# Kernel optimization log

Measured on AMD Instinct MI355X. Metric: run time of the kernel, lower is better.

Reference implementation:

```python
import jax, jax.numpy as jnp
import numpy as np

TEMPERATURE = 0.05
EPS = 1e-8  # torch.cosine_similarity eps


def setup_inputs() -> dict:
    key = jax.random.key(0)
    k1, k2 = jax.random.split(key)
    N, D = 8192, 256
    text_embeddings = jax.random.normal(k1, (N, D), dtype=jnp.float32)
    text_pos_embeddings = jax.random.normal(k2, (N, D), dtype=jnp.float32)
    return {"text_embeddings": text_embeddings, "text_pos_embeddings": text_pos_embeddings}


def reference(text_embeddings, text_pos_embeddings):
    # cosine similarity via normalize + single GEMM (same math as broadcasted
    # torch.cosine_similarity, which clamps norms at eps)
    a_norm = jnp.maximum(jnp.linalg.norm(text_embeddings, axis=-1, keepdims=True), EPS)
    b_norm = jnp.maximum(jnp.linalg.norm(text_pos_embeddings, axis=-1, keepdims=True), EPS)
    a = text_embeddings / a_norm  # [N, D]
    b = text_pos_embeddings / b_norm  # [N, D]
    sim = jnp.einsum("nd,md->nm", a, b) / TEMPERATURE  # [N, N]
    # cross-entropy with labels = arange(N): mean over rows of -log_softmax diag
    logp = jax.nn.log_softmax(sim, axis=-1)
    loss = -jnp.mean(jnp.diagonal(logp))
    return loss
```

## Files before the change

### kernel.cpp

```cpp
#include <hip/hip_runtime.h>
#include <hip/hip_bf16.h>
#include <hip/hip_fp8.h>
#include <math.h>

#define DIM 256

typedef float f32x4 __attribute__((ext_vector_type(4)));
typedef int   i32x8 __attribute__((ext_vector_type(8)));

__constant__ const float kTempInvLog2e = 20.0f * 1.4426950408889634f;
#define LN2 0.6931471805599453f
#define EPS_NORM 1e-8f
#define SCALE_ONE 0x7F7F7F7Fu

static __device__ inline unsigned f2fp8x4(float4 v, float s) {
    __hip_fp8_e4m3 a(v.x * s), b(v.y * s), c(v.z * s), d(v.w * s);
    return (unsigned)a.__x | ((unsigned)b.__x << 8) | ((unsigned)c.__x << 16) | ((unsigned)d.__x << 24);
}

static __device__ inline i32x8 ld_frag32(const void* p0, const void* p1) {
    uint4 a = *(const uint4*)p0;
    uint4 b = *(const uint4*)p1;
    i32x8 v;
    v[0] = a.x; v[1] = a.y; v[2] = a.z; v[3] = a.w;
    v[4] = b.x; v[5] = b.y; v[6] = b.z; v[7] = b.w;
    return v;
}

__global__ __launch_bounds__(256) void normpack_kernel(
    const float* __restrict__ A, const float* __restrict__ B,
    unsigned char* __restrict__ Apk, unsigned char* __restrict__ Bpk,
    float* __restrict__ diag, int n)
{
    __shared__ uint4 lA[256];
    __shared__ uint4 lB[256];
    const int t = threadIdx.x;
    const int rl = t >> 4;
    const int c16 = t & 15;
    const int r = blockIdx.x * 16 + rl;

    const float4* pa = (const float4*)(A + (size_t)r * DIM + c16 * 16);
    const float4* pb = (const float4*)(B + (size_t)r * DIM + c16 * 16);
    float4 a0 = pa[0], a1 = pa[1], a2 = pa[2], a3 = pa[3];
    float4 b0 = pb[0], b1 = pb[1], b2 = pb[2], b3 = pb[3];

    float ssa = a0.x*a0.x + a0.y*a0.y + a0.z*a0.z + a0.w*a0.w
              + a1.x*a1.x + a1.y*a1.y + a1.z*a1.z + a1.w*a1.w
              + a2.x*a2.x + a2.y*a2.y + a2.z*a2.z + a2.w*a2.w
              + a3.x*a3.x + a3.y*a3.y + a3.z*a3.z + a3.w*a3.w;
    float ssb = b0.x*b0.x + b0.y*b0.y + b0.z*b0.z + b0.w*b0.w
              + b1.x*b1.x + b1.y*b1.y + b1.z*b1.z + b1.w*b1.w
              + b2.x*b2.x + b2.y*b2.y + b2.z*b2.z + b2.w*b2.w
              + b3.x*b3.x + b3.y*b3.y + b3.z*b3.z + b3.w*b3.w;
    float dd  = a0.x*b0.x + a0.y*b0.y + a0.z*b0.z + a0.w*b0.w
              + a1.x*b1.x + a1.y*b1.y + a1.z*b1.z + a1.w*b1.w
              + a2.x*b2.x + a2.y*b2.y + a2.z*b2.z + a2.w*b2.w
              + a3.x*b3.x + a3.y*b3.y + a3.z*b3.z + a3.w*b3.w;
#pragma unroll
    for (int m = 1; m < 16; m <<= 1) {
        ssa += __shfl_xor(ssa, m, 64);
        ssb += __shfl_xor(ssb, m, 64);
        dd  += __shfl_xor(dd, m, 64);
    }
    float na = fmaxf(sqrtf(ssa), EPS_NORM);
    float nb = fmaxf(sqrtf(ssb), EPS_NORM);
    float sa = kTempInvLog2e / na;
    float sb = 1.0f / nb;
    if (c16 == 0) diag[r] = dd / (na * nb) * kTempInvLog2e;

    const int u = ((c16 >> 3) << 7) + ((c16 & 1) << 6) + rl + ((c16 & 7) >> 1) * 16;
    uint4 ga, gb;
    ga.x = f2fp8x4(a0, sa); ga.y = f2fp8x4(a1, sa);
    ga.z = f2fp8x4(a2, sa); ga.w = f2fp8x4(a3, sa);
    gb.x = f2fp8x4(b0, sb); gb.y = f2fp8x4(b1, sb);
    gb.z = f2fp8x4(b2, sb); gb.w = f2fp8x4(b3, sb);
    lA[u] = ga; lB[u] = gb;
    __syncthreads();

    ((uint4*)Apk)[(size_t)blockIdx.x * 256 + t] = lA[t];
    ((uint4*)Bpk)[(size_t)blockIdx.x * 256 + t] = lB[t];
}

static __device__ inline void async_copy16(const void* g, void* l) {
    __builtin_amdgcn_global_load_lds(
        (const __attribute__((address_space(1))) unsigned int*)g,
        (__attribute__((address_space(3))) unsigned int*)l, 16, 0, 0);
}

__global__ __launch_bounds__(256, 2) void gemm_lse_kernel(
    const unsigned char* __restrict__ Apk, const unsigned char* __restrict__ Bpk,
    float* __restrict__ partial, int n)
{
    __shared__ char ldsbuf[16384];
    const int lane = threadIdx.x & 63;
    const int w = threadIdx.x >> 6;
    const int c = lane & 15;
    const int q = lane >> 4;

    const int i = blockIdx.x;
    const int split = ((i & 7) << 1) | ((i >> 3) & 1);
    const int rowblk = i >> 4;
    const int rowbase = rowblk * 256 + w * 64;

    i32x8 afrag[4][2];
#pragma unroll
    for (int m = 0; m < 4; ++m) {
        const int AT = rowblk * 16 + w * 4 + m;
#pragma unroll
        for (int kc = 0; kc < 2; ++kc) {
            const char* base = (const char*)Apk + ((size_t)AT * 2 + kc) * 2048 + lane * 16;
            afrag[m][kc] = ld_frag32(base, base + 1024);
        }
    }
#pragma unroll
    for (int m = 0; m < 4; ++m)
#pragma unroll
        for (int kc = 0; kc < 2; ++kc)
            asm volatile("" : "+v"(afrag[m][kc]));

    float sums[16];
#pragma unroll
    for (int s = 0; s < 16; ++s) sums[s] = 0.0f;

    const char* bbase = (const char*)Bpk + (size_t)split * 32 * 4096;
    const int niter = 16;

    {
        const char* src = bbase + w * 2048 + (size_t)lane * 16;
        char* dst = ldsbuf + w * 2048;
        async_copy16(src, dst);
        async_copy16(src + 1024, dst + 1024);
    }
    __syncthreads();

    for (int it = 0; it < niter; ++it) {
        const int cur = it & 1;
        if (it + 1 < niter) {
            const char* src = bbase + (size_t)(it + 1) * 8192 + w * 2048 + (size_t)lane * 16;
            char* dst = ldsbuf + (cur ^ 1) * 8192 + w * 2048;
            async_copy16(src, dst);
            async_copy16(src + 1024, dst + 1024);
        }

        f32x4 acc[4][2];
#pragma unroll
        for (int m = 0; m < 4; ++m)
#pragma unroll
            for (int nc = 0; nc < 2; ++nc)
                acc[m][nc] = (f32x4){0.f, 0.f, 0.f, 0.f};

        const char* lb = ldsbuf + cur * 8192 + (size_t)lane * 16;
#pragma unroll
        for (int nc = 0; nc < 2; ++nc) {
#pragma unroll
            for (int kc = 0; kc < 2; ++kc) {
                const char* p = lb + nc * 4096 + kc * 2048;
                i32x8 bfrag = ld_frag32(p, p + 1024);
#pragma unroll
                for (int m = 0; m < 4; ++m)
                    acc[m][nc] = __builtin_amdgcn_mfma_scale_f32_16x16x128_f8f6f4(
                        afrag[m][kc], bfrag, acc[m][nc],
                        0, 0,
                        0, SCALE_ONE,
                        0, SCALE_ONE);
            }
        }

#pragma unroll
        for (int m = 0; m < 4; ++m)
#pragma unroll
            for (int nc = 0; nc < 2; ++nc)
#pragma unroll
                for (int r = 0; r < 4; ++r)
                    sums[m * 4 + r] += __builtin_amdgcn_exp2f(acc[m][nc][r]);

        __syncthreads();
    }

#pragma unroll
    for (int s = 0; s < 16; ++s) {
        float v = sums[s];
        v += __shfl_xor(v, 1, 64);
        v += __shfl_xor(v, 2, 64);
        v += __shfl_xor(v, 4, 64);
        v += __shfl_xor(v, 8, 64);
        sums[s] = v;
    }
    if (c == 0) {
#pragma unroll
        for (int m = 0; m < 4; ++m)
#pragma unroll
            for (int r = 0; r < 4; ++r)
                partial[(size_t)(rowbase + m * 16 + q * 4 + r) * 16 + split] = sums[m * 4 + r];
    }
}

__global__ __launch_bounds__(256) void row_lse_kernel(
    const float* __restrict__ partial, const float* __restrict__ diag,
    float* __restrict__ bsum, int n)
{
    __shared__ float red[256];
    const int row = blockIdx.x * 256 + threadIdx.x;
    float local = 0.0f;
    if (row < n) {
        const float4* p = (const float4*)(partial + (size_t)row * 16);
        float4 p0 = p[0], p1 = p[1], p2 = p[2], p3 = p[3];
        float s = (p0.x + p0.y + p0.z + p0.w) + (p1.x + p1.y + p1.z + p1.w)
                + (p2.x + p2.y + p2.z + p2.w) + (p3.x + p3.y + p3.z + p3.w);
        local = log2f(s) - diag[row];
    }
    red[threadIdx.x] = local;
    __syncthreads();
    for (int off = 128; off > 0; off >>= 1) {
        if (threadIdx.x < off) red[threadIdx.x] += red[threadIdx.x + off];
        __syncthreads();
    }
    if (threadIdx.x == 0) bsum[blockIdx.x] = red[0];
}

__global__ __launch_bounds__(64) void final_kernel(
    const float* __restrict__ bsum, float* __restrict__ out, int nblocks, int n)
{
    float v = (threadIdx.x < nblocks) ? bsum[threadIdx.x] : 0.0f;
#pragma unroll
    for (int m = 1; m < 64; m <<= 1) v += __shfl_xor(v, m, 64);
    if (threadIdx.x == 0) out[0] = v * (LN2 / (float)n);
}

extern "C" void kernel_launch(void* const* d_in, const int* in_sizes, int n_in,
                              void* d_out, int out_size, void* d_ws, size_t ws_size,
                              hipStream_t stream) {
    const int n = in_sizes[0] / DIM;
    const float* A = (const float*)d_in[0];
    const float* B = (const float*)d_in[1];
    float* out = (float*)d_out;

    unsigned char* Apk = (unsigned char*)d_ws;
    unsigned char* Bpk = Apk + (size_t)n * DIM;
    float* partial = (float*)(Bpk + (size_t)n * DIM);
    float* diag = partial + (size_t)n * 16;
    float* bsum = diag + n;

    normpack_kernel<<<n / 16, 256, 0, stream>>>(A, B, Apk, Bpk, diag, n);

    gemm_lse_kernel<<<(n / 256) * 16, 256, 0, stream>>>(Apk, Bpk, partial, n);

    const int nred = (n + 255) / 256;
    row_lse_kernel<<<nred, 256, 0, stream>>>(partial, diag, bsum, n);
    final_kernel<<<1, 64, 0, stream>>>(bsum, out, nred, n);
}
```

Before: 91.23 us.

## Widen GEMM column tile, use packed fp8 conversion, merge final reductions

The GEMM loop now processes 64 B columns per iteration instead of 32, halving the iteration count and barrier count while doubling LDS per block to 32KB and the accumulator registers. The fp8 packing switches from the HIP fp8 class to the hardware packed-convert builtin. The two tail reduction kernels are merged into a single 1024-thread block to save a launch. The larger register and LDS footprint may reduce occupancy, and the single-block finale uses less parallelism.

```diff
diff --git a/kernel.cpp b/kernel.cpp
--- a/kernel.cpp
+++ b/kernel.cpp
@@ -1,6 +1,5 @@
 #include <hip/hip_runtime.h>
 #include <hip/hip_bf16.h>
-#include <hip/hip_fp8.h>
 #include <math.h>
 
 #define DIM 256
@@ -14,8 +13,10 @@
 #define SCALE_ONE 0x7F7F7F7Fu
 
 static __device__ inline unsigned f2fp8x4(float4 v, float s) {
-    __hip_fp8_e4m3 a(v.x * s), b(v.y * s), c(v.z * s), d(v.w * s);
-    return (unsigned)a.__x | ((unsigned)b.__x << 8) | ((unsigned)c.__x << 16) | ((unsigned)d.__x << 24);
+    int r = 0;
+    r = __builtin_amdgcn_cvt_pk_fp8_f32(v.x * s, v.y * s, r, false);
+    r = __builtin_amdgcn_cvt_pk_fp8_f32(v.z * s, v.w * s, r, true);
+    return (unsigned)r;
 }
 
 static __device__ inline i32x8 ld_frag32(const void* p0, const void* p1) {
@@ -91,7 +92,7 @@
     const unsigned char* __restrict__ Apk, const unsigned char* __restrict__ Bpk,
     float* __restrict__ partial, int n)
 {
-    __shared__ char ldsbuf[16384];
+    __shared__ char ldsbuf[32768];
     const int lane = threadIdx.x & 63;
     const int w = threadIdx.x >> 6;
     const int c = lane & 15;
@@ -123,35 +124,37 @@
     for (int s = 0; s < 16; ++s) sums[s] = 0.0f;
 
     const char* bbase = (const char*)Bpk + (size_t)split * 32 * 4096;
-    const int niter = 16;
+    const int niter = 8;
 
     {
-        const char* src = bbase + w * 2048 + (size_t)lane * 16;
-        char* dst = ldsbuf + w * 2048;
-        async_copy16(src, dst);
-        async_copy16(src + 1024, dst + 1024);
+        const char* src = bbase + w * 4096 + (size_t)lane * 16;
+        char* dst = ldsbuf + w * 4096;
+#pragma unroll
+        for (int j = 0; j < 4; ++j)
+            async_copy16(src + j * 1024, dst + j * 1024);
     }
     __syncthreads();
 
     for (int it = 0; it < niter; ++it) {
         const int cur = it & 1;
         if (it + 1 < niter) {
-            const char* src = bbase + (size_t)(it + 1) * 8192 + w * 2048 + (size_t)lane * 16;
-            char* dst = ldsbuf + (cur ^ 1) * 8192 + w * 2048;
-            async_copy16(src, dst);
-            async_copy16(src + 1024, dst + 1024);
+            const char* src = bbase + (size_t)(it + 1) * 16384 + w * 4096 + (size_t)lane * 16;
+            char* dst = ldsbuf + (cur ^ 1) * 16384 + w * 4096;
+#pragma unroll
+            for (int j = 0; j < 4; ++j)
+                async_copy16(src + j * 1024, dst + j * 1024);
         }
 
-        f32x4 acc[4][2];
+        f32x4 acc[4][4];
 #pragma unroll
         for (int m = 0; m < 4; ++m)
 #pragma unroll
-            for (int nc = 0; nc < 2; ++nc)
+            for (int nc = 0; nc < 4; ++nc)
                 acc[m][nc] = (f32x4){0.f, 0.f, 0.f, 0.f};
 
-        const char* lb = ldsbuf + cur * 8192 + (size_t)lane * 16;
-#pragma unroll
-        for (int nc = 0; nc < 2; ++nc) {
+        const char* lb = ldsbuf + cur * 16384 + (size_t)lane * 16;
+#pragma unroll
+        for (int nc = 0; nc < 4; ++nc) {
 #pragma unroll
             for (int kc = 0; kc < 2; ++kc) {
                 const char* p = lb + nc * 4096 + kc * 2048;
@@ -169,7 +172,7 @@
 #pragma unroll
         for (int m = 0; m < 4; ++m)
 #pragma unroll
-            for (int nc = 0; nc < 2; ++nc)
+            for (int nc = 0; nc < 4; ++nc)
 #pragma unroll
                 for (int r = 0; r < 4; ++r)
                     sums[m * 4 + r] += __builtin_amdgcn_exp2f(acc[m][nc][r]);
@@ -195,36 +198,26 @@
     }
 }
 
-__global__ __launch_bounds__(256) void row_lse_kernel(
+__global__ __launch_bounds__(1024) void finale_kernel(
     const float* __restrict__ partial, const float* __restrict__ diag,
-    float* __restrict__ bsum, int n)
+    float* __restrict__ out, int n)
 {
-    __shared__ float red[256];
-    const int row = blockIdx.x * 256 + threadIdx.x;
+    __shared__ float red[1024];
     float local = 0.0f;
-    if (row < n) {
+    for (int row = threadIdx.x; row < n; row += 1024) {
         const float4* p = (const float4*)(partial + (size_t)row * 16);
         float4 p0 = p[0], p1 = p[1], p2 = p[2], p3 = p[3];
         float s = (p0.x + p0.y + p0.z + p0.w) + (p1.x + p1.y + p1.z + p1.w)
                 + (p2.x + p2.y + p2.z + p2.w) + (p3.x + p3.y + p3.z + p3.w);
-        local = log2f(s) - diag[row];
+        local += log2f(s) - diag[row];
     }
     red[threadIdx.x] = local;
     __syncthreads();
-    for (int off = 128; off > 0; off >>= 1) {
+    for (int off = 512; off > 0; off >>= 1) {
         if (threadIdx.x < off) red[threadIdx.x] += red[threadIdx.x + off];
         __syncthreads();
     }
-    if (threadIdx.x == 0) bsum[blockIdx.x] = red[0];
-}
-
-__global__ __launch_bounds__(64) void final_kernel(
-    const float* __restrict__ bsum, float* __restrict__ out, int nblocks, int n)
-{
-    float v = (threadIdx.x < nblocks) ? bsum[threadIdx.x] : 0.0f;
-#pragma unroll
-    for (int m = 1; m < 64; m <<= 1) v += __shfl_xor(v, m, 64);
-    if (threadIdx.x == 0) out[0] = v * (LN2 / (float)n);
+    if (threadIdx.x == 0) out[0] = red[0] * (LN2 / (float)n);
 }
 
 extern "C" void kernel_launch(void* const* d_in, const int* in_sizes, int n_in,
@@ -239,13 +232,10 @@
     unsigned char* Bpk = Apk + (size_t)n * DIM;
     float* partial = (float*)(Bpk + (size_t)n * DIM);
     float* diag = partial + (size_t)n * 16;
-    float* bsum = diag + n;
 
     normpack_kernel<<<n / 16, 256, 0, stream>>>(A, B, Apk, Bpk, diag, n);
 
     gemm_lse_kernel<<<(n / 256) * 16, 256, 0, stream>>>(Apk, Bpk, partial, n);
 
-    const int nred = (n + 255) / 256;
-    row_lse_kernel<<<nred, 256, 0, stream>>>(partial, diag, bsum, n);
-    final_kernel<<<1, 64, 0, stream>>>(bsum, out, nred, n);
-}
+    finale_kernel<<<1, 1024, 0, stream>>>(partial, diag, out, n);
+}
```

Measured after the change: 96.22 us. +5.5%, slower.
